# Kernel tuning notes

Measured on AMD Instinct MI355X. Metric: run time of the kernel, lower is better.

Reference implementation:

```python
import jax, jax.numpy as jnp
import numpy as np

N_DRUG = 10000
N_DIS = 10000
IN_UNITS = 256
N_EDGES = 1000000


def setup_inputs() -> dict:
    key = jax.random.key(0)
    ks = jax.random.split(key, 10)
    # Kaiming-uniform-ish init like torch Linear defaults
    def lin_w(k, fan_in, fan_out):
        bound = 1.0 / np.sqrt(fan_in)
        return jax.random.uniform(k, (fan_in, fan_out), jnp.float32, -bound, bound)
    return {
        "drug_feat": jax.random.normal(ks[0], (N_DRUG, IN_UNITS), jnp.float32),
        "dis_feat": jax.random.normal(ks[1], (N_DIS, IN_UNITS), jnp.float32),
        "src_idx": jax.random.randint(ks[2], (N_EDGES,), 0, N_DRUG, jnp.int64),
        "dst_idx": jax.random.randint(ks[3], (N_EDGES,), 0, N_DIS, jnp.int64),
        "W1": lin_w(ks[4], 2 * IN_UNITS, 128),
        "b1": jnp.zeros((128,), jnp.float32),
        "W2": lin_w(ks[5], 128, 64),
        "b2": jnp.zeros((64,), jnp.float32),
        "W3": lin_w(ks[6], 64, 1),
        "b3": jnp.zeros((1,), jnp.float32),
    }


def reference(drug_feat, dis_feat, src_idx, dst_idx, W1, b1, W2, b2, W3, b3):
    # apply_edges: gather src (drug) and dst (disease) features, concat -> [E, 2*in_units]
    m = jnp.concatenate([drug_feat[src_idx], dis_feat[dst_idx]], axis=1)
    # 3-layer MLP (dropout = identity in eval)
    h = jax.nn.relu(m @ W1 + b1)
    h = jax.nn.relu(h @ W2 + b2)
    out = h @ W3 + b3  # [E, 1]
    return out
```

## Files before the change

kernel.cpp:

```cpp
#include <hip/hip_runtime.h>
#include <hip/hip_fp16.h>

#define IN_UNITS 256
#define H1 128
#define H2 64

typedef _Float16 f16x8 __attribute__((ext_vector_type(8)));
typedef _Float16 f16x2 __attribute__((ext_vector_type(2)));
typedef float f32x4 __attribute__((ext_vector_type(4)));

union HV { uint4 u; f16x8 v; };

static __device__ __forceinline__ unsigned short h2bits(_Float16 x) {
    union { _Float16 h; unsigned short u; } c; c.h = x; return c.u;
}

#define KEEP4(q) asm volatile("" : "+v"(q.x), "+v"(q.y), "+v"(q.z), "+v"(q.w))

__global__ __launch_bounds__(256) void pack_kernel(
    const float* __restrict__ W1, const float* __restrict__ W2,
    uint4* __restrict__ w1pack, uint4* __restrict__ w2pack)
{
    int b = blockIdx.x, t = threadIdx.x;
    if (b < 4) {
        int item = b * 256 + t;
        int f = item >> 6, l = item & 63;
        int ks = f >> 2, nt = f & 3;
        int row0 = ks * 32 + (l >> 4) * 8;
        int col  = nt * 16 + (l & 15);
        unsigned short h[8];
        #pragma unroll
        for (int j = 0; j < 8; ++j)
            h[j] = h2bits((_Float16)W2[(size_t)(row0 + j) * H2 + col]);
        uint4 v;
        v.x = (unsigned)h[0] | ((unsigned)h[1] << 16);
        v.y = (unsigned)h[2] | ((unsigned)h[3] << 16);
        v.z = (unsigned)h[4] | ((unsigned)h[5] << 16);
        v.w = (unsigned)h[6] | ((unsigned)h[7] << 16);
        w2pack[item] = v;
    } else {
        int idx = (b - 4) * 256 + t;
        int l = idx & 63, f = idx >> 6;
        int nt = f & 3, ch = (f >> 2) & 1, ks = (f >> 3) & 7, side = f >> 6;
        int row0 = side * IN_UNITS + ks * 32 + (l >> 4) * 8;
        int col  = ch * 64 + nt * 16 + (l & 15);
        unsigned short h[8];
        #pragma unroll
        for (int j = 0; j < 8; ++j)
            h[j] = h2bits((_Float16)W1[(size_t)(row0 + j) * H1 + col]);
        uint4 v;
        v.x = (unsigned)h[0] | ((unsigned)h[1] << 16);
        v.y = (unsigned)h[2] | ((unsigned)h[3] << 16);
        v.z = (unsigned)h[4] | ((unsigned)h[5] << 16);
        v.w = (unsigned)h[6] | ((unsigned)h[7] << 16);
        w1pack[idx] = v;
    }
}

__global__ __launch_bounds__(256) __attribute__((amdgpu_waves_per_eu(2, 2)))
void proj_kernel(
    const float* __restrict__ drug_feat, const float* __restrict__ dis_feat,
    const uint4* __restrict__ w1pack, const float* __restrict__ b1,
    unsigned short* __restrict__ drug_h, unsigned short* __restrict__ dis_h,
    int n_rows)
{
    int t = threadIdx.x, lane = t & 63, wave = t >> 6;
    int side = wave >> 1, ch = wave & 1;
    int mtile = blockIdx.x;
    const float* feat = side ? dis_feat : drug_feat;
    unsigned short* outb = side ? dis_h : drug_h;

    int row = mtile * 16 + (lane & 15);
    if (row >= n_rows) row = n_rows - 1;
    int kb = (lane >> 4) * 8;

    float4 fx[16];
    #pragma unroll
    for (int i = 0; i < 16; ++i)
        fx[i] = *(const float4*)(feat + (size_t)row * IN_UNITS + (i >> 1) * 32 + kb + (i & 1) * 4);

    int fbase = side * 64 + ch * 4;
    f32x4 acc[4];
    #pragma unroll
    for (int nt = 0; nt < 4; ++nt) acc[nt] = (f32x4){0.f, 0.f, 0.f, 0.f};

    #pragma unroll
    for (int ks = 0; ks < 8; ++ks) {
        float4 x0 = fx[ks * 2], x1 = fx[ks * 2 + 1];
        f16x8 a;
        a[0] = (_Float16)x0.x; a[1] = (_Float16)x0.y;
        a[2] = (_Float16)x0.z; a[3] = (_Float16)x0.w;
        a[4] = (_Float16)x1.x; a[5] = (_Float16)x1.y;
        a[6] = (_Float16)x1.z; a[7] = (_Float16)x1.w;
        #pragma unroll
        for (int nt = 0; nt < 4; ++nt) {
            HV bb; bb.u = w1pack[(size_t)(fbase + ks * 8 + nt) * 64 + lane];
            acc[nt] = __builtin_amdgcn_mfma_f32_16x16x32_f16(a, bb.v, acc[nt], 0, 0, 0);
        }
    }

    #pragma unroll
    for (int nt = 0; nt < 4; ++nt) {
        int col = ch * 64 + nt * 16 + (lane & 15);
        float bb = side ? b1[col] : 0.f;
        #pragma unroll
        for (int r = 0; r < 4; ++r) {
            int rr = mtile * 16 + (lane >> 4) * 4 + r;
            if (rr < n_rows)
                outb[(size_t)rr * H1 + col] = h2bits((_Float16)(acc[nt][r] + bb));
        }
    }
}

__global__ __launch_bounds__(256) __attribute__((amdgpu_waves_per_eu(3, 3)))
void edge_kernel(
    const unsigned short* __restrict__ drug_h, const unsigned short* __restrict__ dis_h,
    const int* __restrict__ src_idx, const int* __restrict__ dst_idx,
    const uint4* __restrict__ w2pack, const float* __restrict__ b2,
    const float* __restrict__ W3, const float* __restrict__ b3,
    float* __restrict__ out, int n_edges)
{
    __shared__ uint4 w2s[1024];

    int t = threadIdx.x, lane = t & 63, wave = t >> 6;
    int e0 = (blockIdx.x * 4 + wave) * 32;
    int emax = n_edges - 1;

    int i0 = e0 + (lane & 15);      if (i0 > emax) i0 = emax;
    int i1 = e0 + 16 + (lane & 15); if (i1 > emax) i1 = emax;
    int s0 = src_idx[i0], d0 = dst_idx[i0];
    int s1 = src_idx[i1], d1 = dst_idx[i1];

    int kb = (lane >> 4) * 8;
    const uint4* pa0 = (const uint4*)(drug_h + s0 * H1 + kb);
    const uint4* pc0 = (const uint4*)(dis_h  + d0 * H1 + kb);
    const uint4* pa1 = (const uint4*)(drug_h + s1 * H1 + kb);
    const uint4* pc1 = (const uint4*)(dis_h  + d1 * H1 + kb);
    uint4 ga0[4], gc0[4], ga1[4], gc1[4];
    #pragma unroll
    for (int ks = 0; ks < 4; ++ks) {
        ga0[ks] = pa0[ks * 4];
        gc0[ks] = pc0[ks * 4];
        ga1[ks] = pa1[ks * 4];
        gc1[ks] = pc1[ks * 4];
    }

    float b2v[4], w3v[4];
    #pragma unroll
    for (int nt = 0; nt < 4; ++nt) {
        int col = (lane & 15) + nt * 16;
        b2v[nt] = b2[col];
        w3v[nt] = W3[col];
    }
    float b3v = b3[0];

    #pragma unroll
    for (int i = 0; i < 4; ++i) w2s[i * 256 + t] = w2pack[i * 256 + t];

    #pragma unroll
    for (int ks = 0; ks < 4; ++ks) { KEEP4(ga0[ks]); KEEP4(gc0[ks]); KEEP4(ga1[ks]); KEEP4(gc1[ks]); }
    __syncthreads();

    f32x4 acc[2][4];
    #pragma unroll
    for (int mt = 0; mt < 2; ++mt)
        #pragma unroll
        for (int nt = 0; nt < 4; ++nt)
            acc[mt][nt] = (f32x4){0.f, 0.f, 0.f, 0.f};

    #pragma unroll
    for (int ks = 0; ks < 4; ++ks) {
        HV a0, c0, a1, c1;
        a0.u = ga0[ks]; c0.u = gc0[ks];
        a1.u = ga1[ks]; c1.u = gc1[ks];
        f16x8 zero = (f16x8)(_Float16)0;
        f16x8 r0v = __builtin_elementwise_max(a0.v + c0.v, zero);
        f16x8 r1v = __builtin_elementwise_max(a1.v + c1.v, zero);
        #pragma unroll
        for (int nt = 0; nt < 4; ++nt) {
            HV bb; bb.u = w2s[(ks * 4 + nt) * 64 + lane];
            acc[0][nt] = __builtin_amdgcn_mfma_f32_16x16x32_f16(r0v, bb.v, acc[0][nt], 0, 0, 0);
            acc[1][nt] = __builtin_amdgcn_mfma_f32_16x16x32_f16(r1v, bb.v, acc[1][nt], 0, 0, 0);
        }
    }

    #pragma unroll
    for (int mt = 0; mt < 2; ++mt) {
        float part[4];
        #pragma unroll
        for (int r = 0; r < 4; ++r) {
            float p = 0.f;
            #pragma unroll
            for (int nt = 0; nt < 4; ++nt)
                p += fmaxf(acc[mt][nt][r] + b2v[nt], 0.f) * w3v[nt];
            part[r] = p;
        }
        #pragma unroll
        for (int off = 1; off <= 8; off <<= 1)
            #pragma unroll
            for (int r = 0; r < 4; ++r)
                part[r] += __shfl_xor(part[r], off, 64);
        if ((lane & 15) == 0) {
            #pragma unroll
            for (int r = 0; r < 4; ++r) {
                int e = e0 + mt * 16 + (lane >> 4) * 4 + r;
                if (e < n_edges) out[e] = part[r] + b3v;
            }
        }
    }
}

extern "C" void kernel_launch(void* const* d_in, const int* in_sizes, int n_in,
                              void* d_out, int out_size, void* d_ws, size_t ws_size,
                              hipStream_t stream) {
    const float* drug_feat = (const float*)d_in[0];
    const float* dis_feat  = (const float*)d_in[1];
    const int*   src_idx   = (const int*)d_in[2];
    const int*   dst_idx   = (const int*)d_in[3];
    const float* W1 = (const float*)d_in[4];
    const float* b1 = (const float*)d_in[5];
    const float* W2 = (const float*)d_in[6];
    const float* b2 = (const float*)d_in[7];
    const float* W3 = (const float*)d_in[8];
    const float* b3 = (const float*)d_in[9];
    float* out = (float*)d_out;

    int n_edges = in_sizes[2];
    int n_drug = in_sizes[0] / IN_UNITS;

    uint4* w2pack = (uint4*)d_ws;
    uint4* w1pack = (uint4*)((char*)d_ws + 32 * 1024);
    unsigned short* drug_h = (unsigned short*)((char*)d_ws + 192 * 1024);
    unsigned short* dis_h  = drug_h + (size_t)n_drug * H1;

    pack_kernel<<<36, 256, 0, stream>>>(W1, W2, w1pack, w2pack);

    int mtiles = (n_drug + 15) / 16;
    proj_kernel<<<mtiles, 256, 0, stream>>>(
        drug_feat, dis_feat, w1pack, b1, drug_h, dis_h, n_drug);

    int edge_blocks = (n_edges + 127) / 128;
    edge_kernel<<<edge_blocks, 256, 0, stream>>>(
        drug_h, dis_h, src_idx, dst_idx, w2pack, b2, W3, b3, out, n_edges);
}
```

Baseline: 170.9 us.

## Drop weight-packing kernel and convert weights inline in proj and edge kernels

Removes the separate pack_kernel launch. proj_kernel now reads W1 from fp32 global memory with strided scalar loads and converts to fp16 per MFMA fragment. edge_kernel builds the packed W2 tile in shared memory from fp32 W2 in every block. The edge kernel's occupancy hint is also raised from 3 to 6-8 waves per EU and the register-keeping asm barriers are dropped. This saves one launch, but every one of roughly 7800 edge blocks now does 8 scattered fp32 loads per slot to rebuild W2. proj_kernel also issues many uncoalesced W1 loads.

After: 198.1 us. +15.9%, slower.

```diff
diff --git a/kernel.cpp b/kernel.cpp
--- a/kernel.cpp
+++ b/kernel.cpp
@@ -6,61 +6,18 @@
 #define H2 64
 
 typedef _Float16 f16x8 __attribute__((ext_vector_type(8)));
-typedef _Float16 f16x2 __attribute__((ext_vector_type(2)));
 typedef float f32x4 __attribute__((ext_vector_type(4)));
 
-union HV { uint4 u; f16x8 v; };
+union HV { uint4 u; f16x8 v; unsigned short s[8]; };
 
 static __device__ __forceinline__ unsigned short h2bits(_Float16 x) {
     union { _Float16 h; unsigned short u; } c; c.h = x; return c.u;
 }
 
-#define KEEP4(q) asm volatile("" : "+v"(q.x), "+v"(q.y), "+v"(q.z), "+v"(q.w))
-
-__global__ __launch_bounds__(256) void pack_kernel(
-    const float* __restrict__ W1, const float* __restrict__ W2,
-    uint4* __restrict__ w1pack, uint4* __restrict__ w2pack)
-{
-    int b = blockIdx.x, t = threadIdx.x;
-    if (b < 4) {
-        int item = b * 256 + t;
-        int f = item >> 6, l = item & 63;
-        int ks = f >> 2, nt = f & 3;
-        int row0 = ks * 32 + (l >> 4) * 8;
-        int col  = nt * 16 + (l & 15);
-        unsigned short h[8];
-        #pragma unroll
-        for (int j = 0; j < 8; ++j)
-            h[j] = h2bits((_Float16)W2[(size_t)(row0 + j) * H2 + col]);
-        uint4 v;
-        v.x = (unsigned)h[0] | ((unsigned)h[1] << 16);
-        v.y = (unsigned)h[2] | ((unsigned)h[3] << 16);
-        v.z = (unsigned)h[4] | ((unsigned)h[5] << 16);
-        v.w = (unsigned)h[6] | ((unsigned)h[7] << 16);
-        w2pack[item] = v;
-    } else {
-        int idx = (b - 4) * 256 + t;
-        int l = idx & 63, f = idx >> 6;
-        int nt = f & 3, ch = (f >> 2) & 1, ks = (f >> 3) & 7, side = f >> 6;
-        int row0 = side * IN_UNITS + ks * 32 + (l >> 4) * 8;
-        int col  = ch * 64 + nt * 16 + (l & 15);
-        unsigned short h[8];
-        #pragma unroll
-        for (int j = 0; j < 8; ++j)
-            h[j] = h2bits((_Float16)W1[(size_t)(row0 + j) * H1 + col]);
-        uint4 v;
-        v.x = (unsigned)h[0] | ((unsigned)h[1] << 16);
-        v.y = (unsigned)h[2] | ((unsigned)h[3] << 16);
-        v.z = (unsigned)h[4] | ((unsigned)h[5] << 16);
-        v.w = (unsigned)h[6] | ((unsigned)h[7] << 16);
-        w1pack[idx] = v;
-    }
-}
-
-__global__ __launch_bounds__(256) __attribute__((amdgpu_waves_per_eu(2, 2)))
+__global__ __launch_bounds__(256)
 void proj_kernel(
     const float* __restrict__ drug_feat, const float* __restrict__ dis_feat,
-    const uint4* __restrict__ w1pack, const float* __restrict__ b1,
+    const float* __restrict__ W1, const float* __restrict__ b1,
     unsigned short* __restrict__ drug_h, unsigned short* __restrict__ dis_h,
     int n_rows)
 {
@@ -79,7 +36,9 @@
     for (int i = 0; i < 16; ++i)
         fx[i] = *(const float4*)(feat + (size_t)row * IN_UNITS + (i >> 1) * 32 + kb + (i & 1) * 4);
 
-    int fbase = side * 64 + ch * 4;
+    const float* w1base = W1 + (size_t)(side * IN_UNITS + (lane >> 4) * 8) * H1
+                             + ch * 64 + (lane & 15);
+
     f32x4 acc[4];
     #pragma unroll
     for (int nt = 0; nt < 4; ++nt) acc[nt] = (f32x4){0.f, 0.f, 0.f, 0.f};
@@ -94,7 +53,10 @@
         a[6] = (_Float16)x1.z; a[7] = (_Float16)x1.w;
         #pragma unroll
         for (int nt = 0; nt < 4; ++nt) {
-            HV bb; bb.u = w1pack[(size_t)(fbase + ks * 8 + nt) * 64 + lane];
+            HV bb;
+            #pragma unroll
+            for (int j = 0; j < 8; ++j)
+                bb.s[j] = h2bits((_Float16)w1base[(size_t)(ks * 32 + j) * H1 + nt * 16]);
             acc[nt] = __builtin_amdgcn_mfma_f32_16x16x32_f16(a, bb.v, acc[nt], 0, 0, 0);
         }
     }
@@ -112,17 +74,18 @@
     }
 }
 
-__global__ __launch_bounds__(256) __attribute__((amdgpu_waves_per_eu(3, 3)))
+__global__ __launch_bounds__(256) __attribute__((amdgpu_waves_per_eu(6, 8)))
 void edge_kernel(
     const unsigned short* __restrict__ drug_h, const unsigned short* __restrict__ dis_h,
     const int* __restrict__ src_idx, const int* __restrict__ dst_idx,
-    const uint4* __restrict__ w2pack, const float* __restrict__ b2,
+    const float* __restrict__ W2, const float* __restrict__ b2,
     const float* __restrict__ W3, const float* __restrict__ b3,
     float* __restrict__ out, int n_edges)
 {
     __shared__ uint4 w2s[1024];
 
-    int t = threadIdx.x, lane = t & 63, wave = t >> 6;
+    int t = threadIdx.x, lane = t & 63;
+    int wave = t >> 6;
     int e0 = (blockIdx.x * 4 + wave) * 32;
     int emax = n_edges - 1;
 
@@ -130,6 +93,20 @@
     int i1 = e0 + 16 + (lane & 15); if (i1 > emax) i1 = emax;
     int s0 = src_idx[i0], d0 = dst_idx[i0];
     int s1 = src_idx[i1], d1 = dst_idx[i1];
+
+    #pragma unroll
+    for (int i = 0; i < 4; ++i) {
+        int slot = i * 256 + t;
+        int f = slot >> 6, l = slot & 63;
+        int ks = f >> 2, nt = f & 3;
+        int row0 = ks * 32 + (l >> 4) * 8;
+        int col  = nt * 16 + (l & 15);
+        HV v;
+        #pragma unroll
+        for (int j = 0; j < 8; ++j)
+            v.s[j] = h2bits((_Float16)W2[(size_t)(row0 + j) * H2 + col]);
+        w2s[slot] = v.u;
+    }
 
     int kb = (lane >> 4) * 8;
     const uint4* pa0 = (const uint4*)(drug_h + s0 * H1 + kb);
@@ -154,11 +131,6 @@
     }
     float b3v = b3[0];
 
-    #pragma unroll
-    for (int i = 0; i < 4; ++i) w2s[i * 256 + t] = w2pack[i * 256 + t];
-
-    #pragma unroll
-    for (int ks = 0; ks < 4; ++ks) { KEEP4(ga0[ks]); KEEP4(gc0[ks]); KEEP4(ga1[ks]); KEEP4(gc1[ks]); }
     __syncthreads();
 
     f32x4 acc[2][4];
@@ -228,18 +200,14 @@
     int n_edges = in_sizes[2];
     int n_drug = in_sizes[0] / IN_UNITS;
 
-    uint4* w2pack = (uint4*)d_ws;
-    uint4* w1pack = (uint4*)((char*)d_ws + 32 * 1024);
-    unsigned short* drug_h = (unsigned short*)((char*)d_ws + 192 * 1024);
+    unsigned short* drug_h = (unsigned short*)d_ws;
     unsigned short* dis_h  = drug_h + (size_t)n_drug * H1;
-
-    pack_kernel<<<36, 256, 0, stream>>>(W1, W2, w1pack, w2pack);
 
     int mtiles = (n_drug + 15) / 16;
     proj_kernel<<<mtiles, 256, 0, stream>>>(
-        drug_feat, dis_feat, w1pack, b1, drug_h, dis_h, n_drug);
+        drug_feat, dis_feat, W1, b1, drug_h, dis_h, n_drug);
 
     int edge_blocks = (n_edges + 127) / 128;
     edge_kernel<<<edge_blocks, 256, 0, stream>>>(
-        drug_h, dis_h, src_idx, dst_idx, w2pack, b2, W3, b3, out, n_edges);
-}
+        drug_h, dis_h, src_idx, dst_idx, W2, b2, W3, b3, out, n_edges);
+}
```
